# Kernel optimization log

Measured on AMD Instinct MI355X. Metric: run time of the kernel, lower is better.

## Reference

```python
import jax, jax.numpy as jnp
import numpy as np

EMBED_DIM = 2048
NUM_HEADS = 16
NUM_KV_HEADS = 4
KEY_DIM = EMBED_DIM // NUM_HEADS  # 128
B, S = 2, 2048


def setup_inputs() -> dict:
    key = jax.random.key(0)
    ks = jax.random.split(key, 8)
    kv_dim = KEY_DIM * NUM_KV_HEADS
    sc_in = 1.0 / np.sqrt(EMBED_DIM)
    return {
        "query": jax.random.normal(ks[0], (B, S, EMBED_DIM), jnp.float32),
        "key": jax.random.normal(ks[1], (B, S, EMBED_DIM), jnp.float32),
        "value": jax.random.normal(ks[2], (B, S, EMBED_DIM), jnp.float32),
        "mask": jnp.ones((B, S), jnp.float32),
        "Wq": jax.random.normal(ks[3], (EMBED_DIM, EMBED_DIM), jnp.float32) * sc_in,
        "Wk": jax.random.normal(ks[4], (EMBED_DIM, kv_dim), jnp.float32) * sc_in,
        "Wv": jax.random.normal(ks[5], (EMBED_DIM, kv_dim), jnp.float32) * sc_in,
        "Wo": jax.random.normal(ks[6], (EMBED_DIM, EMBED_DIM), jnp.float32) * sc_in,
    }


def reference(query, key, value, mask, Wq, Wk, Wv, Wo):
    b, sq, _ = query.shape
    skv = key.shape[1]
    scale = 1.0 / float(KEY_DIM) ** 0.5
    # projections (no bias)
    q = (query @ Wq).reshape(b, sq, NUM_HEADS, KEY_DIM).transpose(0, 2, 1, 3)      # [B,H,Sq,D]
    k = (key @ Wk).reshape(b, skv, NUM_KV_HEADS, KEY_DIM).transpose(0, 2, 1, 3)    # [B,Hkv,Skv,D]
    v = (value @ Wv).reshape(b, skv, NUM_KV_HEADS, KEY_DIM).transpose(0, 2, 1, 3)  # [B,Hkv,Skv,D]
    n_rep = NUM_HEADS // NUM_KV_HEADS
    k_rep = jnp.repeat(k, n_rep, axis=1)  # [B,H,Skv,D]
    v_rep = jnp.repeat(v, n_rep, axis=1)  # [B,H,Skv,D]
    scores = jnp.einsum("bhqd,bhkd->bhqk", q, k_rep) * scale  # [B,H,Sq,Skv]
    scores = scores + (1.0 - mask[:, None, None, :].astype(scores.dtype)) * -1e9
    attn = jax.nn.softmax(scores, axis=-1)
    out = jnp.einsum("bhqk,bhkd->bhqd", attn, v_rep)  # [B,H,Sq,D]
    out = out.transpose(0, 2, 1, 3).reshape(b, sq, EMBED_DIM)
    return out @ Wo
```

## Files before the change

### kernel.cpp

```cpp
#include <hip/hip_runtime.h>
#include <hip/hip_bf16.h>

#define B_    2
#define S_    2048
#define E_    2048
#define H_    16
#define HKV_  4
#define D_    128
#define NTOK  4096
#define KVDIM 512

typedef __bf16 bf16x8 __attribute__((ext_vector_type(8)));
typedef __bf16 bf16x4 __attribute__((ext_vector_type(4)));
typedef float  f32x4  __attribute__((ext_vector_type(4)));

__device__ __forceinline__ void async_copy16(const void* g, void* l) {
  __builtin_amdgcn_global_load_lds(
      (const __attribute__((address_space(1))) unsigned int*)g,
      (__attribute__((address_space(3))) unsigned int*)l, 16, 0, 0);
}

__global__ __launch_bounds__(256) void cvt_f32_bf16(
    const float* __restrict__ in, __bf16* __restrict__ out, int n) {
  const int i = (blockIdx.x * 256 + threadIdx.x) * 4;
  if (i >= n) return;
  const f32x4 v = *(const f32x4*)(in + i);
  bf16x4 o;
#pragma unroll
  for (int j = 0; j < 4; ++j) o[j] = (__bf16)v[j];
  *(bf16x4*)(out + i) = o;
}

__global__ __launch_bounds__(256) void transpose_f32_bf16(
    const float* __restrict__ in, __bf16* __restrict__ out, int R, int C) {
  __shared__ float t[32][33];
  const int c0 = blockIdx.x * 32;
  const int r0 = blockIdx.y * 32;
  const int tr = threadIdx.x >> 3;
  const int tc = (threadIdx.x & 7) * 4;
  const float* ip = in + (size_t)(r0 + tr) * C + c0 + tc;
#pragma unroll
  for (int i = 0; i < 4; ++i) t[tr][tc + i] = ip[i];
  __syncthreads();
  __bf16* op = out + (size_t)(c0 + tr) * R + r0 + tc;
#pragma unroll
  for (int i = 0; i < 4; ++i) op[i] = (__bf16)t[tc + i][tr];
}

template <int EPI>
__global__ __launch_bounds__(256, 2) void gemm_bt(
    const __bf16* __restrict__ A, const __bf16* __restrict__ Bt,
    void* __restrict__ Cout, int M, int N, int K) {
  __shared__ __align__(16) __bf16 As[128 * 32];
  __shared__ __align__(16) __bf16 Bs[128 * 32];
  const int m0 = blockIdx.y * 128;
  const int n0 = blockIdx.x * 128;
  const int tid = threadIdx.x;
  const int w = tid >> 6;
  const int lane = tid & 63;
  const int quad = lane >> 4;
  const int l16 = lane & 15;
  const int wr = w >> 1, wc = w & 1;
  const int arow = lane >> 2;
  const int acol = (lane & 3) * 8;

  f32x4 acc[4][4] = {};

  for (int k0 = 0; k0 < K; k0 += 32) {
    __syncthreads();
#pragma unroll
    for (int c = 0; c < 2; ++c) {
      const int chunk = w * 2 + c;
      const int row = chunk * 16 + arow;
      async_copy16(A + (size_t)(m0 + row) * K + k0 + acol, &As[chunk * 512]);
      async_copy16(Bt + (size_t)(n0 + row) * K + k0 + acol, &Bs[chunk * 512]);
    }
    __syncthreads();
    bf16x8 af[4], bfr[4];
#pragma unroll
    for (int i = 0; i < 4; ++i)
      af[i] = *(const bf16x8*)&As[(wr * 64 + i * 16 + l16) * 32 + quad * 8];
#pragma unroll
    for (int j = 0; j < 4; ++j)
      bfr[j] = *(const bf16x8*)&Bs[(wc * 64 + j * 16 + l16) * 32 + quad * 8];
#pragma unroll
    for (int i = 0; i < 4; ++i)
#pragma unroll
      for (int j = 0; j < 4; ++j)
        acc[i][j] = __builtin_amdgcn_mfma_f32_16x16x32_bf16(af[i], bfr[j],
                                                            acc[i][j], 0, 0, 0);
  }

#pragma unroll
  for (int i = 0; i < 4; ++i) {
#pragma unroll
    for (int j = 0; j < 4; ++j) {
#pragma unroll
      for (int r = 0; r < 4; ++r) {
        const int m = m0 + wr * 64 + i * 16 + quad * 4 + r;
        const int n = n0 + wc * 64 + j * 16 + l16;
        if (EPI == 0) {
          ((__bf16*)Cout)[(size_t)m * N + n] = (__bf16)acc[i][j][r];
        } else if (EPI == 1) {
          const int b = m >> 11, s = m & (S_ - 1);
          ((__bf16*)Cout)[((size_t)((b * HKV_ + (n >> 7)) * D_ +
                                    (n & (D_ - 1)))) * S_ + s] =
              (__bf16)acc[i][j][r];
        } else {
          ((float*)Cout)[(size_t)m * N + n] = acc[i][j][r];
        }
      }
    }
  }
}

__global__ __launch_bounds__(256, 2) void attn_kernel(
    const __bf16* __restrict__ Q, const __bf16* __restrict__ Kp,
    const __bf16* __restrict__ Vt, const float* __restrict__ mask,
    __bf16* __restrict__ Oa) {
  __shared__ __align__(16) __bf16 K_lds[64][136];
  __shared__ __align__(16) __bf16 V_lds[128][72];
  __shared__ __align__(16) __bf16 P_lds[4][32][72];

  const int tid = threadIdx.x;
  const int w = tid >> 6, lane = tid & 63, quad = lane >> 4, l16 = lane & 15;
  const int bh = blockIdx.y;
  const int b = bh >> 4, h = bh & 15, hkv = h >> 2;
  const int q0 = blockIdx.x * 128 + w * 32;

  const __bf16* qbase = Q + (size_t)(b * S_ + q0) * E_ + h * D_;
  bf16x8 qf[2][4];
#pragma unroll
  for (int m = 0; m < 2; ++m)
#pragma unroll
    for (int ks = 0; ks < 4; ++ks)
      qf[m][ks] = *(const bf16x8*)(qbase + (size_t)(m * 16 + l16) * E_ +
                                   ks * 32 + quad * 8);

  const __bf16* kbase = Kp + (size_t)(b * S_) * KVDIM + hkv * D_;
  const __bf16* vbase = Vt + (size_t)((b * HKV_ + hkv) * D_) * S_;
  const float* mbase = mask + b * S_;

  f32x4 o[2][8] = {};
  f32x4 lsum[2] = {};
  const float scale = 0.08838834764831845f;

  for (int kt = 0; kt < S_; kt += 64) {
    __syncthreads();
#pragma unroll
    for (int i = 0; i < 4; ++i) {
      const int r = w * 16 + i * 4 + (lane >> 4);
      bf16x8 kv = *(const bf16x8*)(kbase + (size_t)(kt + r) * KVDIM +
                                   (lane & 15) * 8);
      *(bf16x8*)&K_lds[r][(lane & 15) * 8] = kv;
    }
#pragma unroll
    for (int i = 0; i < 4; ++i) {
      const int r = w * 32 + i * 8 + (lane >> 3);
      bf16x8 vv = *(const bf16x8*)(vbase + (size_t)r * S_ + kt +
                                   (lane & 7) * 8);
      *(bf16x8*)&V_lds[r][(lane & 7) * 8] = vv;
    }
    __syncthreads();

    f32x4 s[2][4] = {};
#pragma unroll
    for (int ks = 0; ks < 4; ++ks) {
#pragma unroll
      for (int n = 0; n < 4; ++n) {
        bf16x8 kf = *(const bf16x8*)&K_lds[n * 16 + l16][ks * 32 + quad * 8];
        s[0][n] = __builtin_amdgcn_mfma_f32_16x16x32_bf16(qf[0][ks], kf,
                                                          s[0][n], 0, 0, 0);
        s[1][n] = __builtin_amdgcn_mfma_f32_16x16x32_bf16(qf[1][ks], kf,
                                                          s[1][n], 0, 0, 0);
      }
    }

    float bias[4];
#pragma unroll
    for (int n = 0; n < 4; ++n)
      bias[n] = (1.0f - mbase[kt + n * 16 + l16]) * -1e9f;
#pragma unroll
    for (int m = 0; m < 2; ++m) {
#pragma unroll
      for (int n = 0; n < 4; ++n) {
#pragma unroll
        for (int r = 0; r < 4; ++r) {
          const float p = __expf(s[m][n][r] * scale + bias[n]);
          lsum[m][r] += p;
          P_lds[w][m * 16 + quad * 4 + r][n * 16 + l16] = (__bf16)p;
        }
      }
    }

#pragma unroll
    for (int ks2 = 0; ks2 < 2; ++ks2) {
      bf16x8 pa[2];
#pragma unroll
      for (int m = 0; m < 2; ++m)
        pa[m] = *(const bf16x8*)&P_lds[w][m * 16 + l16][ks2 * 32 + quad * 8];
#pragma unroll
      for (int dt = 0; dt < 8; ++dt) {
        bf16x8 vf = *(const bf16x8*)&V_lds[dt * 16 + l16][ks2 * 32 + quad * 8];
        o[0][dt] = __builtin_amdgcn_mfma_f32_16x16x32_bf16(pa[0], vf,
                                                           o[0][dt], 0, 0, 0);
        o[1][dt] = __builtin_amdgcn_mfma_f32_16x16x32_bf16(pa[1], vf,
                                                           o[1][dt], 0, 0, 0);
      }
    }
  }

  __bf16* obase = Oa + (size_t)(b * S_ + q0) * E_ + h * D_;
#pragma unroll
  for (int m = 0; m < 2; ++m) {
#pragma unroll
    for (int r = 0; r < 4; ++r) {
      float v = lsum[m][r];
#pragma unroll
      for (int off = 1; off < 16; off <<= 1) v += __shfl_xor(v, off);
      const float inv = 1.0f / v;
#pragma unroll
      for (int dt = 0; dt < 8; ++dt)
        obase[(size_t)(m * 16 + quad * 4 + r) * E_ + dt * 16 + l16] =
            (__bf16)(o[m][dt][r] * inv);
    }
  }
}

extern "C" void kernel_launch(void* const* d_in, const int* in_sizes, int n_in,
                              void* d_out, int out_size, void* d_ws,
                              size_t ws_size, hipStream_t stream) {
  const float* query = (const float*)d_in[0];
  const float* key   = (const float*)d_in[1];
  const float* value = (const float*)d_in[2];
  const float* mask  = (const float*)d_in[3];
  const float* Wq    = (const float*)d_in[4];
  const float* Wk    = (const float*)d_in[5];
  const float* Wv    = (const float*)d_in[6];
  const float* Wo    = (const float*)d_in[7];
  float* out = (float*)d_out;

  __bf16* ws  = (__bf16*)d_ws;
  __bf16* Xbf = ws;
  __bf16* WT  = Xbf + (size_t)NTOK * E_;
  __bf16* Qp  = WT + (size_t)E_ * E_;
  __bf16* Kp  = Qp + (size_t)NTOK * E_;
  __bf16* Vt  = Kp + (size_t)NTOK * KVDIM;

  const int nA = NTOK * E_;

  cvt_f32_bf16<<<nA / 1024, 256, 0, stream>>>(query, Xbf, nA);
  transpose_f32_bf16<<<dim3(E_ / 32, E_ / 32), 256, 0, stream>>>(Wq, WT, E_, E_);
  gemm_bt<0><<<dim3(E_ / 128, NTOK / 128), 256, 0, stream>>>(
      Xbf, WT, Qp, NTOK, E_, E_);

  cvt_f32_bf16<<<nA / 1024, 256, 0, stream>>>(key, Xbf, nA);
  transpose_f32_bf16<<<dim3(KVDIM / 32, E_ / 32), 256, 0, stream>>>(Wk, WT, E_, KVDIM);
  gemm_bt<0><<<dim3(KVDIM / 128, NTOK / 128), 256, 0, stream>>>(
      Xbf, WT, Kp, NTOK, KVDIM, E_);

  cvt_f32_bf16<<<nA / 1024, 256, 0, stream>>>(value, Xbf, nA);
  transpose_f32_bf16<<<dim3(KVDIM / 32, E_ / 32), 256, 0, stream>>>(Wv, WT, E_, KVDIM);
  gemm_bt<1><<<dim3(KVDIM / 128, NTOK / 128), 256, 0, stream>>>(
      Xbf, WT, Vt, NTOK, KVDIM, E_);

  attn_kernel<<<dim3(S_ / 128, B_ * H_), 256, 0, stream>>>(Qp, Kp, Vt, mask, Xbf);

  transpose_f32_bf16<<<dim3(E_ / 32, E_ / 32), 256, 0, stream>>>(Wo, WT, E_, E_);
  gemm_bt<2><<<dim3(E_ / 128, NTOK / 128), 256, 0, stream>>>(
      Xbf, WT, out, NTOK, E_, E_);
}
```

Before: 455.6 us.

## Fuse activation fp32-to-bf16 conversion into a single merged QKV projection GEMM

Removes the separate fp32-to-bf16 conversion passes by reading fp32 activations directly in the GEMM A-tile load and converting in registers. Merges the Q, K and V projection GEMMs into one launch that dispatches on blockIdx.x, and batches all four weight transposes into one launch. This cuts kernel launches and the round trip of bf16 activation copies through memory. In exchange, A loads become synchronous fp32 global reads (twice the bytes) instead of async LDS copies, and the workspace layout changes, with the attention output aliasing the Wq/Wk/Wv transposed buffers.

```diff
diff --git a/kernel.cpp b/kernel.cpp
--- a/kernel.cpp
+++ b/kernel.cpp
@@ -20,37 +20,126 @@
       (__attribute__((address_space(3))) unsigned int*)l, 16, 0, 0);
 }
 
-__global__ __launch_bounds__(256) void cvt_f32_bf16(
-    const float* __restrict__ in, __bf16* __restrict__ out, int n) {
-  const int i = (blockIdx.x * 256 + threadIdx.x) * 4;
-  if (i >= n) return;
-  const f32x4 v = *(const f32x4*)(in + i);
-  bf16x4 o;
-#pragma unroll
-  for (int j = 0; j < 4; ++j) o[j] = (__bf16)v[j];
-  *(bf16x4*)(out + i) = o;
-}
-
-__global__ __launch_bounds__(256) void transpose_f32_bf16(
-    const float* __restrict__ in, __bf16* __restrict__ out, int R, int C) {
+__global__ __launch_bounds__(256) void transpose_all(
+    const float* __restrict__ Wq, const float* __restrict__ Wk,
+    const float* __restrict__ Wv, const float* __restrict__ Wo,
+    __bf16* __restrict__ WTq, __bf16* __restrict__ WTk,
+    __bf16* __restrict__ WTv, __bf16* __restrict__ WoT) {
+  const float* in;
+  __bf16* out;
+  int C;
+  switch (blockIdx.z) {
+    case 0:  in = Wq; out = WTq; C = E_;   break;
+    case 1:  in = Wk; out = WTk; C = KVDIM; break;
+    case 2:  in = Wv; out = WTv; C = KVDIM; break;
+    default: in = Wo; out = WoT; C = E_;   break;
+  }
+  const int c0 = blockIdx.x * 32;
+  if (c0 >= C) return;
+  const int r0 = blockIdx.y * 32;
   __shared__ float t[32][33];
-  const int c0 = blockIdx.x * 32;
-  const int r0 = blockIdx.y * 32;
   const int tr = threadIdx.x >> 3;
   const int tc = (threadIdx.x & 7) * 4;
   const float* ip = in + (size_t)(r0 + tr) * C + c0 + tc;
 #pragma unroll
   for (int i = 0; i < 4; ++i) t[tr][tc + i] = ip[i];
   __syncthreads();
-  __bf16* op = out + (size_t)(c0 + tr) * R + r0 + tc;
+  __bf16* op = out + (size_t)(c0 + tr) * E_ + r0 + tc;
 #pragma unroll
   for (int i = 0; i < 4; ++i) op[i] = (__bf16)t[tc + i][tr];
 }
 
-template <int EPI>
-__global__ __launch_bounds__(256, 2) void gemm_bt(
+__global__ __launch_bounds__(256, 2) void gemm_qkv(
+    const float* __restrict__ query, const float* __restrict__ key,
+    const float* __restrict__ value, const __bf16* __restrict__ WTq,
+    const __bf16* __restrict__ WTk, const __bf16* __restrict__ WTv,
+    __bf16* __restrict__ Qp, __bf16* __restrict__ Kp,
+    __bf16* __restrict__ Vt) {
+  __shared__ __align__(16) __bf16 As[128 * 32];
+  __shared__ __align__(16) __bf16 Bs[128 * 32];
+
+  const int bx = blockIdx.x;
+  const float* A;
+  const __bf16* Bt;
+  int n0, N, epi;
+  if (bx < 16)      { A = query; Bt = WTq; n0 = bx * 128;        N = E_;    epi = 0; }
+  else if (bx < 20) { A = key;   Bt = WTk; n0 = (bx - 16) * 128; N = KVDIM; epi = 0; }
+  else              { A = value; Bt = WTv; n0 = (bx - 20) * 128; N = KVDIM; epi = 1; }
+  const int m0 = blockIdx.y * 128;
+  const int K = E_;
+
+  const int tid = threadIdx.x;
+  const int w = tid >> 6;
+  const int lane = tid & 63;
+  const int quad = lane >> 4;
+  const int l16 = lane & 15;
+  const int wr = w >> 1, wc = w & 1;
+  const int brow = lane >> 2;
+  const int bcol = (lane & 3) * 8;
+  const int arow = lane >> 2;
+  const int acol = (lane & 3) * 8;
+
+  f32x4 acc[4][4] = {};
+
+  for (int k0 = 0; k0 < K; k0 += 32) {
+    __syncthreads();
+#pragma unroll
+    for (int c = 0; c < 2; ++c) {
+      const int chunk = w * 2 + c;
+      const int row = chunk * 16 + brow;
+      async_copy16(Bt + (size_t)(n0 + row) * K + k0 + bcol, &Bs[chunk * 512]);
+    }
+#pragma unroll
+    for (int s = 0; s < 2; ++s) {
+      const int row = w * 32 + s * 16 + arow;
+      const float* src = A + (size_t)(m0 + row) * K + k0 + acol;
+      const f32x4 a0 = *(const f32x4*)src;
+      const f32x4 a1 = *(const f32x4*)(src + 4);
+      bf16x8 v;
+#pragma unroll
+      for (int j = 0; j < 4; ++j) { v[j] = (__bf16)a0[j]; v[4 + j] = (__bf16)a1[j]; }
+      *(bf16x8*)&As[row * 32 + acol] = v;
+    }
+    __syncthreads();
+    bf16x8 af[4], bfr[4];
+#pragma unroll
+    for (int i = 0; i < 4; ++i)
+      af[i] = *(const bf16x8*)&As[(wr * 64 + i * 16 + l16) * 32 + quad * 8];
+#pragma unroll
+    for (int j = 0; j < 4; ++j)
+      bfr[j] = *(const bf16x8*)&Bs[(wc * 64 + j * 16 + l16) * 32 + quad * 8];
+#pragma unroll
+    for (int i = 0; i < 4; ++i)
+#pragma unroll
+      for (int j = 0; j < 4; ++j)
+        acc[i][j] = __builtin_amdgcn_mfma_f32_16x16x32_bf16(af[i], bfr[j],
+                                                            acc[i][j], 0, 0, 0);
+  }
+
+#pragma unroll
+  for (int i = 0; i < 4; ++i) {
+#pragma unroll
+    for (int j = 0; j < 4; ++j) {
+#pragma unroll
+      for (int r = 0; r < 4; ++r) {
+        const int m = m0 + wr * 64 + i * 16 + quad * 4 + r;
+        const int n = n0 + wc * 64 + j * 16 + l16;
+        if (epi == 0) {
+          __bf16* C = (bx < 16) ? Qp : Kp;
+          C[(size_t)m * N + n] = (__bf16)acc[i][j][r];
+        } else {
+          const int b = m >> 11, s = m & (S_ - 1);
+          Vt[((size_t)((b * HKV_ + (n >> 7)) * D_ + (n & (D_ - 1)))) * S_ + s] =
+              (__bf16)acc[i][j][r];
+        }
+      }
+    }
+  }
+}
+
+__global__ __launch_bounds__(256, 2) void gemm_o(
     const __bf16* __restrict__ A, const __bf16* __restrict__ Bt,
-    void* __restrict__ Cout, int M, int N, int K) {
+    float* __restrict__ Cout, int M, int N, int K) {
   __shared__ __align__(16) __bf16 As[128 * 32];
   __shared__ __align__(16) __bf16 Bs[128 * 32];
   const int m0 = blockIdx.y * 128;
@@ -92,26 +181,15 @@
   }
 
 #pragma unroll
-  for (int i = 0; i < 4; ++i) {
-#pragma unroll
-    for (int j = 0; j < 4; ++j) {
+  for (int i = 0; i < 4; ++i)
+#pragma unroll
+    for (int j = 0; j < 4; ++j)
 #pragma unroll
       for (int r = 0; r < 4; ++r) {
         const int m = m0 + wr * 64 + i * 16 + quad * 4 + r;
         const int n = n0 + wc * 64 + j * 16 + l16;
-        if (EPI == 0) {
-          ((__bf16*)Cout)[(size_t)m * N + n] = (__bf16)acc[i][j][r];
-        } else if (EPI == 1) {
-          const int b = m >> 11, s = m & (S_ - 1);
-          ((__bf16*)Cout)[((size_t)((b * HKV_ + (n >> 7)) * D_ +
-                                    (n & (D_ - 1)))) * S_ + s] =
-              (__bf16)acc[i][j][r];
-        } else {
-          ((float*)Cout)[(size_t)m * N + n] = acc[i][j][r];
-        }
-      }
-    }
-  }
+        Cout[(size_t)m * N + n] = acc[i][j][r];
+      }
 }
 
 __global__ __launch_bounds__(256, 2) void attn_kernel(
@@ -240,33 +318,22 @@
   const float* Wo    = (const float*)d_in[7];
   float* out = (float*)d_out;
 
-  __bf16* ws  = (__bf16*)d_ws;
-  __bf16* Xbf = ws;
-  __bf16* WT  = Xbf + (size_t)NTOK * E_;
-  __bf16* Qp  = WT + (size_t)E_ * E_;
-  __bf16* Kp  = Qp + (size_t)NTOK * E_;
-  __bf16* Vt  = Kp + (size_t)NTOK * KVDIM;
-
-  const int nA = NTOK * E_;
-
-  cvt_f32_bf16<<<nA / 1024, 256, 0, stream>>>(query, Xbf, nA);
-  transpose_f32_bf16<<<dim3(E_ / 32, E_ / 32), 256, 0, stream>>>(Wq, WT, E_, E_);
-  gemm_bt<0><<<dim3(E_ / 128, NTOK / 128), 256, 0, stream>>>(
-      Xbf, WT, Qp, NTOK, E_, E_);
-
-  cvt_f32_bf16<<<nA / 1024, 256, 0, stream>>>(key, Xbf, nA);
-  transpose_f32_bf16<<<dim3(KVDIM / 32, E_ / 32), 256, 0, stream>>>(Wk, WT, E_, KVDIM);
-  gemm_bt<0><<<dim3(KVDIM / 128, NTOK / 128), 256, 0, stream>>>(
-      Xbf, WT, Kp, NTOK, KVDIM, E_);
-
-  cvt_f32_bf16<<<nA / 1024, 256, 0, stream>>>(value, Xbf, nA);
-  transpose_f32_bf16<<<dim3(KVDIM / 32, E_ / 32), 256, 0, stream>>>(Wv, WT, E_, KVDIM);
-  gemm_bt<1><<<dim3(KVDIM / 128, NTOK / 128), 256, 0, stream>>>(
-      Xbf, WT, Vt, NTOK, KVDIM, E_);
-
-  attn_kernel<<<dim3(S_ / 128, B_ * H_), 256, 0, stream>>>(Qp, Kp, Vt, mask, Xbf);
-
-  transpose_f32_bf16<<<dim3(E_ / 32, E_ / 32), 256, 0, stream>>>(Wo, WT, E_, E_);
-  gemm_bt<2><<<dim3(E_ / 128, NTOK / 128), 256, 0, stream>>>(
-      Xbf, WT, out, NTOK, E_, E_);
-}
+  __bf16* ws   = (__bf16*)d_ws;
+  __bf16* Qp   = ws;
+  __bf16* Kp   = Qp + (size_t)NTOK * E_;
+  __bf16* Vt   = Kp + (size_t)NTOK * KVDIM;
+  __bf16* WoT  = Vt + (size_t)NTOK * KVDIM;
+  __bf16* WTq  = WoT + (size_t)E_ * E_;
+  __bf16* WTk  = WTq + (size_t)E_ * E_;
+  __bf16* WTv  = WTk + (size_t)KVDIM * E_;
+  __bf16* Attn = WTq;
+
+  transpose_all<<<dim3(64, 64, 4), 256, 0, stream>>>(Wq, Wk, Wv, Wo,
+                                                     WTq, WTk, WTv, WoT);
+  gemm_qkv<<<dim3(24, 32), 256, 0, stream>>>(query, key, value,
+                                             WTq, WTk, WTv, Qp, Kp, Vt);
+  attn_kernel<<<dim3(S_ / 128, B_ * H_), 256, 0, stream>>>(Qp, Kp, Vt, mask,
+                                                           Attn);
+  gemm_o<<<dim3(E_ / 128, NTOK / 128), 256, 0, stream>>>(Attn, WoT, out,
+                                                         NTOK, E_, E_);
+}
```

After: 402.3 us. -11.7%, faster.
